# Optimization experiments

Hardware: AMD Instinct MI355X
Metric: run time of the kernel (lower is better)

## Reference

```python
import jax, jax.numpy as jnp
import numpy as np

D_MODEL = 2048
N_HEAD = 16
HEAD_DIM = D_MODEL // N_HEAD


def setup_inputs() -> dict:
    key = jax.random.key(0)
    k1, k2, k3 = jax.random.split(key, 3)
    B, T = 4, 1024
    x = jax.random.normal(k1, (B, T, D_MODEL), dtype=jnp.float32)
    # Linear(d_model, 3*d_model, bias=False): stored as [in, out] for x @ W
    w_qkv = jax.random.normal(k2, (D_MODEL, 3 * D_MODEL), dtype=jnp.float32) * (1.0 / np.sqrt(D_MODEL))
    w_proj = jax.random.normal(k3, (D_MODEL, D_MODEL), dtype=jnp.float32) * (1.0 / np.sqrt(D_MODEL))
    return {"x": x, "w_qkv": w_qkv, "w_proj": w_proj}


def reference(x, w_qkv, w_proj):
    B, T, C = x.shape
    H, Dh = N_HEAD, HEAD_DIM
    qkv = x @ w_qkv                              # [B, T, 3C]
    q, k, v = jnp.split(qkv, 3, axis=-1)
    # [B, T, C] -> [B, H, T, Dh]
    q = q.reshape(B, T, H, Dh).transpose(0, 2, 1, 3)
    k = k.reshape(B, T, H, Dh).transpose(0, 2, 1, 3)
    v = v.reshape(B, T, H, Dh).transpose(0, 2, 1, 3)
    scale = 1.0 / np.sqrt(Dh).astype(np.float32)
    scores = jnp.einsum('bhqd,bhkd->bhqk', q, k) * scale   # [B, H, T, T]
    causal = jnp.tril(jnp.ones((T, T), dtype=bool))
    scores = jnp.where(causal, scores, jnp.finfo(scores.dtype).min)
    attn = jax.nn.softmax(scores, axis=-1)
    y = jnp.einsum('bhqk,bhkd->bhqd', attn, v)             # [B, H, T, Dh]
    y = y.transpose(0, 2, 1, 3).reshape(B, T, C)
    return y @ w_proj
```

## Files before the change

kernel.cpp:

```cpp
#include <hip/hip_runtime.h>
#include <cstdint>
#include <cstddef>


typedef __attribute__((ext_vector_type(8))) __bf16 bf16x8;
typedef __attribute__((ext_vector_type(4))) float f32x4;
typedef unsigned short u16;

#define NEG_BIG (-1.0e30f)

__device__ __forceinline__ u16 f2bf(float f) {
    union { float f; uint32_t u; } v; v.f = f;
    uint32_t r = v.u + 0x7FFFu + ((v.u >> 16) & 1u);
    return (u16)(r >> 16);
}

__device__ __forceinline__ uint32_t pack2(float a, float b) {
    return (uint32_t)f2bf(a) | ((uint32_t)f2bf(b) << 16);
}

__device__ __forceinline__ f32x4 mfma16(bf16x8 a, bf16x8 b, f32x4 c) {
    return __builtin_amdgcn_mfma_f32_16x16x32_bf16(a, b, c, 0, 0, 0);
}

__device__ __forceinline__ void async16(const u16* g, u16* l) {
    __builtin_amdgcn_global_load_lds(
        (const __attribute__((address_space(1))) void*)g,
        (__attribute__((address_space(3))) void*)l, 16, 0, 0);
}

__global__ __launch_bounds__(256) void cvt_bf16(
    const float* __restrict__ x, u16* __restrict__ xb) {
    size_t i = ((size_t)blockIdx.x * 256 + threadIdx.x) * 8;
    float4 u = *(const float4*)(x + i);
    float4 v = *(const float4*)(x + i + 4);
    uint4 p;
    p.x = pack2(u.x, u.y); p.y = pack2(u.z, u.w);
    p.z = pack2(v.x, v.y); p.w = pack2(v.z, v.w);
    *(uint4*)(xb + i) = p;
}

__global__ __launch_bounds__(256) void transpose_w(
    const float* __restrict__ W, int ldW, u16* __restrict__ WT) {
    __shared__ u16 tile[64][68];
    const int n0 = blockIdx.x * 64, k0 = blockIdx.y * 64;
    const int t = threadIdx.x;
    for (int i = t; i < 4096; i += 256) {
        int r = i >> 6, c = i & 63;
        tile[r][c] = f2bf(W[(size_t)(k0 + r) * ldW + n0 + c]);
    }
    __syncthreads();
    for (int i = t; i < 4096; i += 256) {
        int r = i >> 6, c = i & 63;
        WT[(size_t)(n0 + r) * 2048 + k0 + c] = tile[c][r];
    }
}

__global__ __launch_bounds__(256) void gemm_k(
    const void* __restrict__ Av, const u16* __restrict__ Bt,
    int N, int amode, int omode,
    float* __restrict__ outf, u16* __restrict__ Qo, u16* __restrict__ Ko,
    u16* __restrict__ Vt) {
    const int K = 2048;
    __shared__ u16 As[128][32];
    __shared__ u16 Bs[128][32];

    const float* A32 = (const float*)Av;
    const u16*   A16 = (const u16*)Av;

    const int m0 = blockIdx.y * 128, n0 = blockIdx.x * 128;
    const int t = threadIdx.x;
    const int w = t >> 6, lane = t & 63;
    const int col = lane & 15, quad = lane >> 4;
    const int wrow = (w >> 1) * 64, wcol = (w & 1) * 64;

    f32x4 acc[4][4];
    #pragma unroll
    for (int i = 0; i < 4; ++i)
        #pragma unroll
        for (int j = 0; j < 4; ++j)
            acc[i][j] = (f32x4){0.f, 0.f, 0.f, 0.f};

    u16* as_flat = &As[0][0];
    u16* bs_flat = &Bs[0][0];
    const int c1 = (w << 6) | lane;
    const int c2 = c1 + 256;

    for (int k0 = 0; k0 < K; k0 += 32) {
        {
            const u16* g1 = Bt + (size_t)(n0 + (c1 >> 2)) * K + k0 + ((c1 & 3) << 3);
            async16(g1, bs_flat + (size_t)w * 512);
            const u16* g2 = Bt + (size_t)(n0 + (c2 >> 2)) * K + k0 + ((c2 & 3) << 3);
            async16(g2, bs_flat + 2048 + (size_t)w * 512);
        }
        if (amode == 2) {
            const u16* g1 = A16 + (size_t)(m0 + (c1 >> 2)) * K + k0 + ((c1 & 3) << 3);
            async16(g1, as_flat + (size_t)w * 512);
            const u16* g2 = A16 + (size_t)(m0 + (c2 >> 2)) * K + k0 + ((c2 & 3) << 3);
            async16(g2, as_flat + 2048 + (size_t)w * 512);
        } else if (amode == 1) {
            #pragma unroll
            for (int cc = 0; cc < 2; ++cc) {
                int c = cc ? c2 : c1;
                int r = c >> 2, ko = (c & 3) << 3;
                int kg = k0 + ko, h = kg >> 7, d = kg & 127;
                int m = m0 + r, b = m >> 10, tt = m & 1023;
                const u16* g = A16 + (((size_t)(b * 16 + h)) * 1024 + tt) * 128 + d;
                async16(g, as_flat + (size_t)(cc ? 2048 : 0) + (size_t)w * 512);
            }
        } else if (amode == 0) {
            #pragma unroll
            for (int c = t; c < 512; c += 256) {
                int r = c >> 2, ko = (c & 3) * 8;
                size_t off = (size_t)(m0 + r) * K + k0 + ko;
                float4 u = *(const float4*)(A32 + off);
                float4 v = *(const float4*)(A32 + off + 4);
                uint4 p;
                p.x = pack2(u.x, u.y); p.y = pack2(u.z, u.w);
                p.z = pack2(v.x, v.y); p.w = pack2(v.z, v.w);
                *(uint4*)&As[r][ko] = p;
            }
        } else {
            #pragma unroll
            for (int c = t; c < 512; c += 256) {
                int r = c >> 2, ko = (c & 3) * 8;
                int kg = k0 + ko, h = kg >> 7, d = kg & 127;
                int m = m0 + r, b = m >> 10, tt = m & 1023;
                *(uint4*)&As[r][ko] =
                    *(const uint4*)(A16 + (((size_t)(b * 16 + h)) * 1024 + tt) * 128 + d);
            }
        }
        __syncthreads();

        bf16x8 afr[4], bfr[4];
        #pragma unroll
        for (int i = 0; i < 4; ++i)
            afr[i] = *(const bf16x8*)&As[wrow + i * 16 + col][quad * 8];
        #pragma unroll
        for (int i = 0; i < 4; ++i)
            bfr[i] = *(const bf16x8*)&Bs[wcol + i * 16 + col][quad * 8];

        #pragma unroll
        for (int mt = 0; mt < 4; ++mt)
            #pragma unroll
            for (int nt = 0; nt < 4; ++nt)
                acc[mt][nt] = mfma16(afr[mt], bfr[nt], acc[mt][nt]);
        __syncthreads();
    }

    #pragma unroll
    for (int mt = 0; mt < 4; ++mt) {
        #pragma unroll
        for (int nt = 0; nt < 4; ++nt) {
            #pragma unroll
            for (int r = 0; r < 4; ++r) {
                int gm = m0 + wrow + mt * 16 + quad * 4 + r;
                int gn = n0 + wcol + nt * 16 + col;
                if (omode == 0) {
                    outf[(size_t)gm * N + gn] = acc[mt][nt][r];
                } else {
                    u16 bv = f2bf(acc[mt][nt][r]);
                    int b = gm >> 10, tq = gm & 1023;
                    if (omode == 3) {
                        int which = gn >> 11, rem = gn & 2047;
                        int h = rem >> 7, d = rem & 127;
                        size_t bh = (size_t)b * 16 + h;
                        if (which == 0)      Qo[(bh * 1024 + tq) * 128 + d] = bv;
                        else if (which == 1) Ko[(bh * 1024 + tq) * 128 + d] = bv;
                        else                 Vt[(bh * 128 + d) * 1024 + tq] = bv;
                    } else {
                        int h = gn >> 7, d = gn & 127;
                        size_t bh = (size_t)b * 16 + h;
                        if (omode == 1) Qo[(bh * 1024 + tq) * 128 + d] = bv;
                        else            Vt[(bh * 128 + d) * 1024 + tq] = bv;
                    }
                }
            }
        }
    }
}

__device__ __forceinline__ bf16x8 ldsfrag(const u16* buf, int row, int ksl, int quad) {
    return *(const bf16x8*)(buf + (size_t)row * 64 +
                            ((((ksl << 2) | quad) ^ (row & 7)) << 3));
}

__device__ __forceinline__ void stage64(
    u16* dst, const u16* src, int row0, int k0, int w, int lane) {
    int s = (w << 6) | lane;
    int r = s >> 3;
    int gc = (s & 7) ^ (r & 7);
    async16(src + (size_t)(row0 + r) * 2048 + k0 + (gc << 3),
            dst + ((size_t)(w << 6)) * 8);
}

__global__ __launch_bounds__(512, 2) void gemm192(
    const u16* __restrict__ A, const u16* __restrict__ Bt,
    u16* __restrict__ Qo, u16* __restrict__ Ko, u16* __restrict__ Vt) {
    __shared__ u16 As[2][256 * 64];
    __shared__ u16 Bs[2][192 * 64];

    const int m0 = blockIdx.y * 256, n0 = blockIdx.x * 192;
    const int t = threadIdx.x;
    const int w = t >> 6, lane = t & 63;
    const int col = lane & 15, quad = lane >> 4;
    const int wr16 = ((w >> 2) & 1) << 4;
    const int wc48 = (w & 3) * 48;

    f32x4 acc[8][3];
    #pragma unroll
    for (int i = 0; i < 8; ++i)
        #pragma unroll
        for (int j = 0; j < 3; ++j)
            acc[i][j] = (f32x4){0.f, 0.f, 0.f, 0.f};

    stage64(Bs[0] + 0 * 4096,  Bt, n0 + 0,   0, w, lane);
    stage64(Bs[0] + 1 * 4096,  Bt, n0 + 64,  0, w, lane);
    stage64(Bs[0] + 2 * 4096,  Bt, n0 + 128, 0, w, lane);
    stage64(As[0] + 0 * 4096,  A,  m0 + 0,   0, w, lane);
    stage64(As[0] + 1 * 4096,  A,  m0 + 64,  0, w, lane);
    stage64(As[0] + 2 * 4096,  A,  m0 + 128, 0, w, lane);
    stage64(As[0] + 3 * 4096,  A,  m0 + 192, 0, w, lane);

    bf16x8 af[8], bfc[6];
    const int NT = 32;

    for (int kt = 0; kt < NT; ++kt) {
        const int cur = kt & 1, nxt = cur ^ 1;
        const int kN = ((kt + 1) & 31) * 64;

        asm volatile("s_waitcnt vmcnt(2)" ::: "memory");
        __builtin_amdgcn_s_barrier();
        #pragma unroll
        for (int mr = 0; mr < 4; ++mr)
            #pragma unroll
            for (int ks = 0; ks < 2; ++ks)
                af[mr * 2 + ks] = ldsfrag(As[cur], mr * 32 + wr16 + col, ks, quad);
        #pragma unroll
        for (int nt = 0; nt < 3; ++nt)
            #pragma unroll
            for (int ks = 0; ks < 2; ++ks)
                bfc[nt * 2 + ks] = ldsfrag(Bs[cur], wc48 + nt * 16 + col, ks, quad);
        stage64(Bs[nxt] + 0 * 4096, Bt, n0 + 0,   kN, w, lane);
        stage64(Bs[nxt] + 1 * 4096, Bt, n0 + 64,  kN, w, lane);
        stage64(Bs[nxt] + 2 * 4096, Bt, n0 + 128, kN, w, lane);
        __builtin_amdgcn_s_setprio(1);
        #pragma unroll
        for (int mr = 0; mr < 4; ++mr)
            #pragma unroll
            for (int nt = 0; nt < 3; ++nt)
                #pragma unroll
                for (int ks = 0; ks < 2; ++ks)
                    acc[mr][nt] = mfma16(af[mr * 2 + ks], bfc[nt * 2 + ks], acc[mr][nt]);
        __builtin_amdgcn_s_setprio(0);

        asm volatile("s_waitcnt vmcnt(3)" ::: "memory");
        __builtin_amdgcn_s_barrier();
        #pragma unroll
        for (int mr = 0; mr < 4; ++mr)
            #pragma unroll
            for (int ks = 0; ks < 2; ++ks)
                af[mr * 2 + ks] = ldsfrag(As[cur], (mr + 4) * 32 + wr16 + col, ks, quad);
        stage64(As[nxt] + 0 * 4096, A, m0 + 0,   kN, w, lane);
        stage64(As[nxt] + 1 * 4096, A, m0 + 64,  kN, w, lane);
        stage64(As[nxt] + 2 * 4096, A, m0 + 128, kN, w, lane);
        stage64(As[nxt] + 3 * 4096, A, m0 + 192, kN, w, lane);
        __builtin_amdgcn_s_setprio(1);
        #pragma unroll
        for (int mr = 0; mr < 4; ++mr)
            #pragma unroll
            for (int nt = 0; nt < 3; ++nt)
                #pragma unroll
                for (int ks = 0; ks < 2; ++ks)
                    acc[mr + 4][nt] = mfma16(af[mr * 2 + ks], bfc[nt * 2 + ks], acc[mr + 4][nt]);
        __builtin_amdgcn_s_setprio(0);
    }

    #pragma unroll
    for (int mr = 0; mr < 8; ++mr) {
        #pragma unroll
        for (int nt = 0; nt < 3; ++nt) {
            #pragma unroll
            for (int r = 0; r < 4; ++r) {
                int gm = m0 + mr * 32 + wr16 + quad * 4 + r;
                int gn = n0 + wc48 + nt * 16 + col;
                u16 bv = f2bf(acc[mr][nt][r]);
                int b = gm >> 10, tq = gm & 1023;
                int which = gn >> 11, rem = gn & 2047;
                int hh = rem >> 7, d = rem & 127;
                size_t bh = (size_t)b * 16 + hh;
                if (which == 0)      Qo[(bh * 1024 + tq) * 128 + d] = bv;
                else if (which == 1) Ko[(bh * 1024 + tq) * 128 + d] = bv;
                else                 Vt[(bh * 128 + d) * 1024 + tq] = bv;
            }
        }
    }
}

__global__ __launch_bounds__(256) void attn_kernel(
    u16* __restrict__ Q, const u16* __restrict__ K,
    const u16* __restrict__ VT) {
    __shared__ u16 Ks[64 * 128];
    __shared__ u16 Vs[128 * 64];
    __shared__ u16 Ps[4][16][68];

    const int bx = (int)blockIdx.x;
    const int h = blockIdx.y, b = blockIdx.z;
    const int t = threadIdx.x;
    const int w = t >> 6, lane = t & 63;
    const int col = lane & 15, quad = lane >> 4;
    const int sw = col & 7;
    const size_t bh = (size_t)b * 16 + h;
    u16* Qb = Q + bh * (1024 * 128);
    const u16* Kb = K + bh * (1024 * 128);
    const u16* Vb = VT + bh * (128 * 1024);
    const float scale = 0.08838834764831845f;

    #pragma unroll 1
    for (int qs = 0; qs < 2; ++qs) {
        const int qb = qs ? bx : 15 - bx;
        const int q_lane = qb * 64 + w * 16 + col;

        bf16x8 qf[4];
        {
            const u16* qp = Qb + (size_t)q_lane * 128 + quad * 8;
            #pragma unroll
            for (int kq = 0; kq < 4; ++kq)
                qf[kq] = *(const bf16x8*)(qp + kq * 32);
        }

        f32x4 o[8];
        #pragma unroll
        for (int i = 0; i < 8; ++i) o[i] = (f32x4){0.f, 0.f, 0.f, 0.f};
        float m = NEG_BIG, l = 0.f;

        for (int kt = 0; kt <= qb; ++kt) {
            const u16* Kt = Kb + (size_t)kt * (64 * 128);

            #pragma unroll
            for (int i = 0; i < 4; ++i) {
                int s = i * 256 + w * 64 + lane;
                int kr = s >> 4, kc = s & 15;
                async16(Kt + (size_t)kr * 128 + ((kc ^ (kr & 7)) << 3),
                        Ks + (size_t)(i * 256 + w * 64) * 8);
                int vr = s >> 3, vc = s & 7;
                async16(Vb + (size_t)vr * 1024 + kt * 64 + ((vc ^ (vr & 7)) << 3),
                        Vs + (size_t)(i * 256 + w * 64) * 8);
            }
            __syncthreads();

            const bool need_mask = (kt == qb);
            const int ttmax = need_mask ? w : 3;
            f32x4 s[4];
            #pragma unroll
            for (int tt = 0; tt < 4; ++tt) {
                if (tt > ttmax) { s[tt] = (f32x4){NEG_BIG, NEG_BIG, NEG_BIG, NEG_BIG}; continue; }
                const u16* kbase = Ks + (size_t)(tt * 16 + col) * 128;
                f32x4 a = (f32x4){0.f, 0.f, 0.f, 0.f};
                #pragma unroll
                for (int kq = 0; kq < 4; ++kq)
                    a = mfma16(*(const bf16x8*)(kbase + (((kq * 4 + quad) ^ sw) << 3)),
                               qf[kq], a);
                s[tt] = a;
            }

            float rmax = NEG_BIG;
            #pragma unroll
            for (int tt = 0; tt < 4; ++tt) {
                if (tt > ttmax) continue;
                #pragma unroll
                for (int r = 0; r < 4; ++r) {
                    float v = s[tt][r] * scale;
                    int tg = kt * 64 + tt * 16 + quad * 4 + r;
                    if (need_mask && tg > q_lane) v = NEG_BIG;
                    s[tt][r] = v;
                    rmax = fmaxf(rmax, v);
                }
            }
            rmax = fmaxf(rmax, __shfl_xor(rmax, 16, 64));
            rmax = fmaxf(rmax, __shfl_xor(rmax, 32, 64));

            float mnew = fmaxf(m, rmax);
            float alpha = __expf(m - mnew);
            m = mnew;

            float rsum = 0.f;
            #pragma unroll
            for (int tt = 0; tt < 4; ++tt) {
                uint32_t* dst = (uint32_t*)&Ps[w][col][tt * 16 + quad * 4];
                if (tt > ttmax) { dst[0] = 0u; dst[1] = 0u; continue; }
                float p0 = __expf(s[tt][0] - mnew);
                float p1 = __expf(s[tt][1] - mnew);
                float p2 = __expf(s[tt][2] - mnew);
                float p3 = __expf(s[tt][3] - mnew);
                rsum += (p0 + p1) + (p2 + p3);
                dst[0] = pack2(p0, p1);
                dst[1] = pack2(p2, p3);
            }
            rsum += __shfl_xor(rsum, 16, 64);
            rsum += __shfl_xor(rsum, 32, 64);
            l = l * alpha + rsum;

            #pragma unroll
            for (int dt = 0; dt < 8; ++dt)
                #pragma unroll
                for (int r = 0; r < 4; ++r) o[dt][r] *= alpha;

            #pragma unroll
            for (int ks = 0; ks < 2; ++ks) {
                bf16x8 pf = *(const bf16x8*)&Ps[w][col][ks * 32 + quad * 8];
                #pragma unroll
                for (int dt = 0; dt < 8; ++dt) {
                    const u16* vbase = Vs + (size_t)(dt * 16 + col) * 64;
                    o[dt] = mfma16(*(const bf16x8*)(vbase + (((ks * 4 + quad) ^ sw) << 3)),
                                   pf, o[dt]);
                }
            }
            __syncthreads();
        }

        float inv = 1.0f / l;
        #pragma unroll
        for (int dt = 0; dt < 8; ++dt) {
            uint2 p;
            p.x = pack2(o[dt][0] * inv, o[dt][1] * inv);
            p.y = pack2(o[dt][2] * inv, o[dt][3] * inv);
            *(uint2*)&Qb[(size_t)q_lane * 128 + dt * 16 + quad * 4] = p;
        }
    }
}

extern "C" void kernel_launch(void* const* d_in, const int* in_sizes, int n_in,
                              void* d_out, int out_size, void* d_ws, size_t ws_size,
                              hipStream_t stream) {
    const float* x      = (const float*)d_in[0];
    const float* w_qkv  = (const float*)d_in[1];
    const float* w_proj = (const float*)d_in[2];
    float* out = (float*)d_out;

    const size_t SEG = (size_t)4 * 16 * 1024 * 128;
    const size_t NEED_FAST = ((size_t)6144 * 2048 + SEG * 4) * 2;

    if (ws_size >= NEED_FAST + (1u << 20)) {
        u16* wT = (u16*)d_ws;
        u16* xb = wT + (size_t)6144 * 2048;
        u16* Qb = xb + SEG;
        u16* Kb = Qb + SEG;
        u16* Vb = Kb + SEG;

        cvt_bf16<<<4096, 256, 0, stream>>>(x, xb);
        transpose_w<<<dim3(96, 32), 256, 0, stream>>>(w_qkv, 6144, wT);

        gemm192<<<dim3(32, 16), 512, 0, stream>>>(xb, wT, Qb, Kb, Vb);

        attn_kernel<<<dim3(8, 16, 4), 256, 0, stream>>>(Qb, Kb, Vb);

        transpose_w<<<dim3(32, 32), 256, 0, stream>>>(w_proj, 2048, wT);
        gemm_k<<<dim3(16, 32), 256, 0, stream>>>(Qb, wT, 2048, 1, 0,
                                                 out, nullptr, nullptr, nullptr);
    } else {
        u16* wT = (u16*)d_ws;
        u16* Qb = wT + (size_t)2048 * 2048;
        u16* Kb = Qb + SEG;
        u16* Vb = Kb + SEG;

        transpose_w<<<dim3(32, 32), 256, 0, stream>>>(w_qkv + 0, 6144, wT);
        gemm_k<<<dim3(16, 32), 256, 0, stream>>>(x, wT, 2048, 0, 1,
                                                 nullptr, Qb, nullptr, nullptr);
        transpose_w<<<dim3(32, 32), 256, 0, stream>>>(w_qkv + 2048, 6144, wT);
        gemm_k<<<dim3(16, 32), 256, 0, stream>>>(x, wT, 2048, 0, 1,
                                                 nullptr, Kb, nullptr, nullptr);
        transpose_w<<<dim3(32, 32), 256, 0, stream>>>(w_qkv + 4096, 6144, wT);
        gemm_k<<<dim3(16, 32), 256, 0, stream>>>(x, wT, 2048, 0, 2,
                                                 nullptr, nullptr, nullptr, Vb);

        attn_kernel<<<dim3(8, 16, 4), 256, 0, stream>>>(Qb, Kb, Vb);

        transpose_w<<<dim3(32, 32), 256, 0, stream>>>(w_proj, 2048, wT);
        gemm_k<<<dim3(16, 32), 256, 0, stream>>>(Qb, wT, 2048, 3, 0,
                                                 out, nullptr, nullptr, nullptr);
    }
}
```

Baseline: 372.6 us.

## Double-buffer K/V tiles in attention kernel to overlap loads with compute

Splits the shared K and V tiles into two buffers and prefetches the next KV tile with async loads while the current tile is being computed. Partial vmcnt waits plus raw barriers replace the full __syncthreads before compute. The aim is to hide global-memory latency behind the MFMA work. In exchange, LDS use doubles, which may lower occupancy, and correctness now depends on the vmcnt(8) count matching the eight async loads issued per stage.

```diff
diff --git a/kernel.cpp b/kernel.cpp
--- a/kernel.cpp
+++ b/kernel.cpp
@@ -297,11 +297,26 @@
     }
 }
 
+__device__ __forceinline__ void stage_kv(
+    u16* KsB, u16* VsB, const u16* Kt, const u16* Vb, int kvoff,
+    int w, int lane) {
+    #pragma unroll
+    for (int i = 0; i < 4; ++i) {
+        int s = i * 256 + w * 64 + lane;
+        int kr = s >> 4, kc = s & 15;
+        async16(Kt + (size_t)kr * 128 + ((kc ^ (kr & 7)) << 3),
+                KsB + (size_t)(i * 256 + w * 64) * 8);
+        int vr = s >> 3, vc = s & 7;
+        async16(Vb + (size_t)vr * 1024 + kvoff + ((vc ^ (vr & 7)) << 3),
+                VsB + (size_t)(i * 256 + w * 64) * 8);
+    }
+}
+
 __global__ __launch_bounds__(256) void attn_kernel(
     u16* __restrict__ Q, const u16* __restrict__ K,
     const u16* __restrict__ VT) {
-    __shared__ u16 Ks[64 * 128];
-    __shared__ u16 Vs[128 * 64];
+    __shared__ u16 Ks[2][64 * 128];
+    __shared__ u16 Vs[2][128 * 64];
     __shared__ u16 Ps[4][16][68];
 
     const int bx = (int)blockIdx.x;
@@ -334,20 +349,22 @@
         for (int i = 0; i < 8; ++i) o[i] = (f32x4){0.f, 0.f, 0.f, 0.f};
         float m = NEG_BIG, l = 0.f;
 
+        stage_kv(Ks[0], Vs[0], Kb, Vb, 0, w, lane);
+        asm volatile("s_waitcnt vmcnt(0)" ::: "memory");
+        __builtin_amdgcn_s_barrier();
+
         for (int kt = 0; kt <= qb; ++kt) {
-            const u16* Kt = Kb + (size_t)kt * (64 * 128);
-
-            #pragma unroll
-            for (int i = 0; i < 4; ++i) {
-                int s = i * 256 + w * 64 + lane;
-                int kr = s >> 4, kc = s & 15;
-                async16(Kt + (size_t)kr * 128 + ((kc ^ (kr & 7)) << 3),
-                        Ks + (size_t)(i * 256 + w * 64) * 8);
-                int vr = s >> 3, vc = s & 7;
-                async16(Vb + (size_t)vr * 1024 + kt * 64 + ((vc ^ (vr & 7)) << 3),
-                        Vs + (size_t)(i * 256 + w * 64) * 8);
-            }
-            __syncthreads();
+            const int cur = kt & 1, nxt = cur ^ 1;
+
+            if (kt < qb) {
+                stage_kv(Ks[nxt], Vs[nxt],
+                         Kb + (size_t)(kt + 1) * (64 * 128), Vb,
+                         (kt + 1) * 64, w, lane);
+                asm volatile("s_waitcnt vmcnt(8)" ::: "memory");
+            } else {
+                asm volatile("s_waitcnt vmcnt(0)" ::: "memory");
+            }
+            __builtin_amdgcn_s_barrier();
 
             const bool need_mask = (kt == qb);
             const int ttmax = need_mask ? w : 3;
@@ -355,7 +372,7 @@
             #pragma unroll
             for (int tt = 0; tt < 4; ++tt) {
                 if (tt > ttmax) { s[tt] = (f32x4){NEG_BIG, NEG_BIG, NEG_BIG, NEG_BIG}; continue; }
-                const u16* kbase = Ks + (size_t)(tt * 16 + col) * 128;
+                const u16* kbase = Ks[cur] + (size_t)(tt * 16 + col) * 128;
                 f32x4 a = (f32x4){0.f, 0.f, 0.f, 0.f};
                 #pragma unroll
                 for (int kq = 0; kq < 4; ++kq)
@@ -411,12 +428,12 @@
                 bf16x8 pf = *(const bf16x8*)&Ps[w][col][ks * 32 + quad * 8];
                 #pragma unroll
                 for (int dt = 0; dt < 8; ++dt) {
-                    const u16* vbase = Vs + (size_t)(dt * 16 + col) * 64;
+                    const u16* vbase = Vs[cur] + (size_t)(dt * 16 + col) * 64;
                     o[dt] = mfma16(*(const bf16x8*)(vbase + (((ks * 4 + quad) ^ sw) << 3)),
                                    pf, o[dt]);
                 }
             }
-            __syncthreads();
+            __builtin_amdgcn_s_barrier();
         }
 
         float inv = 1.0f / l;
```

Result: no change. 377.1 us (+1.2%).
